# Kernel optimization log

Measured on AMD Instinct MI355X. Metric: run time of the kernel, lower is better.

Reference implementation:

```python
import jax, jax.numpy as jnp
import numpy as np
from jax import lax


def _forward(z_real, z_imag, dt, conv_w, conv_b, lin_w, lin_b,
             sc_w1, sc_b1, sc_w2, sc_b2, L_gen, diss_base, viscosity):
    B, T, C, H, W = z_real.shape
    Wf = W // 2 + 1
    x_mag = jnp.sqrt(z_real * z_real + z_imag * z_imag)  # |z|, (B,T,C,H,W)

    # ---- CFLTimeWarper ----
    v_proxy = x_mag.mean(axis=(3, 4), keepdims=True) + 1e-6      # (B,T,C,1,1)
    dt_max = 1.0 / (v_proxy * 10.0)                              # dx=1, max_velocity=10
    x_in = jnp.concatenate([z_real, z_imag], axis=2).reshape(B * T, 2 * C, H, W)
    h = lax.conv_general_dilated(x_in, conv_w, (1, 1), 'SAME',
                                 dimension_numbers=('NCHW', 'OIHW', 'NCHW'))
    h = jax.nn.silu(h + conv_b[None, :, None, None])
    pooled = h.mean(axis=(2, 3))                                 # AdaptiveAvgPool2d(1)
    alpha = jax.nn.sigmoid(pooled @ lin_w.T + lin_b).reshape(B, T, 1, 1, 1)
    dt_eff = alpha * jnp.minimum(dt, dt_max)                     # (B,T,C,1,1)

    # ---- LyapunovController (out_dim = 3C) ----
    ge = x_mag.mean(axis=(-2, -1))                               # (B,T,C)
    ctrl = jnp.tanh(jax.nn.silu(ge @ sc_w1.T + sc_b1) @ sc_w2.T + sc_b2)  # (B,T,3C)
    d_omega = ctrl[..., :C] * 0.1
    valve = ctrl[..., 2 * C:]
    omega_t = L_gen + d_omega                                    # (B,T,C)
    B_valve = jax.nn.sigmoid(valve) * 2.0                        # (B,T,C)

    # ---- spectral decay / rotation operators ----
    gamma_base = -jax.nn.softplus(diss_base)                     # (C,)
    nu = jax.nn.softplus(viscosity)
    ky = jnp.fft.fftfreq(H).astype(jnp.float32)
    kx = jnp.fft.rfftfreq(W).astype(jnp.float32)
    k_sq = kx[None, :] ** 2 + ky[:, None] ** 2                   # (H,Wf)
    gamma_k = gamma_base[:, None, None] - nu * k_sq[None]        # (C,H,Wf)
    gamma_term = gamma_k[None, None] * dt_eff                    # (B,T,C,H,Wf)
    omega_term = omega_t[..., None, None] * dt_eff               # (B,T,C,1,1)
    A_decay = jnp.exp(gamma_term)
    half = 0.5j * omega_term.astype(jnp.complex64)
    A_rot = (1.0 + half) / (1.0 - half)                          # Cayley rotation
    A_op = A_decay * A_rot                                       # (B,T,C,H,Wf) complex

    # ---- forward_spectral: complex input -> stack real/imag on batch ----
    u_in = jnp.concatenate([z_real, z_imag], axis=0)             # (2B,T,C,H,W)
    A_op = jnp.concatenate([A_op, A_op], axis=0)                 # (2B,T,C,H,Wf)
    Bv = jnp.concatenate([B_valve, B_valve], axis=0)             # (2B,T,C)
    z_fft = jnp.fft.rfft2(u_in, norm='ortho')                    # (2B,T,C,H,Wf)
    u_fft = z_fft * Bv[..., None, None]
    u_flat = jnp.transpose(u_fft, (0, 3, 4, 1, 2)).reshape(2 * B * H * Wf, T, C)
    A_flat = jnp.transpose(A_op, (0, 3, 4, 1, 2)).reshape(2 * B * H * Wf, T, C)
    return u_flat, A_flat, dt_eff


def setup_inputs() -> dict:
    key = jax.random.key(0)
    ks = jax.random.split(key, 10)
    B, T, C, H, W = 2, 8, 64, 128, 128
    z_real = jax.random.normal(ks[0], (B, T, C, H, W), jnp.float32)
    z_imag = jax.random.normal(ks[1], (B, T, C, H, W), jnp.float32)
    dt = jnp.ones((), jnp.float32)
    conv_w = jax.random.normal(ks[2], (C // 4, 2 * C, 3, 3), jnp.float32) * 0.05
    conv_b = jnp.zeros((C // 4,), jnp.float32)
    lin_w = jax.random.normal(ks[3], (1, C // 4), jnp.float32) * 0.05
    lin_b = jnp.zeros((1,), jnp.float32)
    sc_w1 = jax.random.normal(ks[4], (C // 2, C), jnp.float32) * 0.05
    sc_b1 = jnp.zeros((C // 2,), jnp.float32)
    sc_w2 = jax.random.normal(ks[5], (3 * C, C // 2), jnp.float32) * 0.05
    sc_b2 = jnp.zeros((3 * C,), jnp.float32)
    L_gen = jax.random.normal(ks[6], (C,), jnp.float32) * 0.01
    diss_base = jnp.zeros((C,), jnp.float32)
    viscosity = jnp.float32(0.001)
    return {"z_real": z_real, "z_imag": z_imag, "dt": dt,
            "conv_w": conv_w, "conv_b": conv_b, "lin_w": lin_w, "lin_b": lin_b,
            "sc_w1": sc_w1, "sc_b1": sc_b1, "sc_w2": sc_w2, "sc_b2": sc_b2,
            "L_gen": L_gen, "diss_base": diss_base, "viscosity": viscosity}


def reference(z_real, z_imag, dt, conv_w, conv_b, lin_w, lin_b,
              sc_w1, sc_b1, sc_w2, sc_b2, L_gen, diss_base, viscosity):
    return _forward(z_real, z_imag, dt, conv_w, conv_b, lin_w, lin_b,
                    sc_w1, sc_b1, sc_w2, sc_b2, L_gen, diss_base, viscosity)
```

## Files before the change

kernel.cpp:

```cpp
#include <hip/hip_runtime.h>
#include <math.h>

#define HW_ 16384

#define WS_GE    0
#define WS_POOL  1024
#define WS_DTEFF 17408
#define WS_ROTRE 18432
#define WS_ROTIM 19456
#define WS_BV    20480
#define WS_GB    21504
#define WS_NU    21568
__device__ float g_ws[22528];


struct Tw {
  float t0c, t0s;
  float c[6], s[6];
};

__device__ __forceinline__ void tw_init(int lane, Tw& tw) {
  sincospif(-(float)lane * (1.0f / 64.0f), &tw.t0s, &tw.t0c);
#pragma unroll
  for (int i = 0; i < 6; ++i) {
    int sp = 32 >> i;
    int j = lane & (sp - 1);
    float sv, cv;
    sincospif(-(float)j / (float)sp, &sv, &cv);
    bool bit = (lane & sp) != 0;
    tw.c[i] = bit ? cv : 1.0f;
    tw.s[i] = bit ? sv : 0.0f;
  }
}

__device__ __forceinline__ void fft128(int lane, float2& e0, float2& e1, const Tw& tw) {
  float ax = e0.x + e1.x, ay = e0.y + e1.y;
  float dx = e0.x - e1.x, dy = e0.y - e1.y;
  e0.x = ax; e0.y = ay;
  float t1x = dx * tw.t0c - dy * tw.t0s;
  float t1y = dx * tw.t0s + dy * tw.t0c;
  e1.x = t1x; e1.y = t1y;
#pragma unroll
  for (int i = 0; i < 6; ++i) {
    int sp = 32 >> i;
    bool bit = (lane & sp) != 0;
    float o0x = __shfl_xor(e0.x, sp, 64);
    float o0y = __shfl_xor(e0.y, sp, 64);
    float o1x = __shfl_xor(e1.x, sp, 64);
    float o1y = __shfl_xor(e1.y, sp, 64);
    float s0x = bit ? (o0x - e0.x) : (e0.x + o0x);
    float s0y = bit ? (o0y - e0.y) : (e0.y + o0y);
    float s1x = bit ? (o1x - e1.x) : (e1.x + o1x);
    float s1y = bit ? (o1y - e1.y) : (e1.y + o1y);
    e0.x = s0x * tw.c[i] - s0y * tw.s[i];
    e0.y = s0x * tw.s[i] + s0y * tw.c[i];
    e1.x = s1x * tw.c[i] - s1y * tw.s[i];
    e1.y = s1x * tw.s[i] + s1y * tw.c[i];
  }
}

__global__ __launch_bounds__(256) void k_rowfft2(
    const float* __restrict__ zsrc, const float* __restrict__ zother,
    float2* __restrict__ panel, int with_mag)
{
  __shared__ __align__(16) float2 Mr[65][34];
  __shared__ __align__(16) float2 Wb[4][128];
  __shared__ float redb[4];

  int n = blockIdx.x;
  int b = n >> 9, t = (n >> 6) & 7, c = n & 63;
  int tid = threadIdx.x, w = tid >> 6, lane = tid & 63;
  const float* pr = zsrc + (size_t)n * HW_;
  const float* po = zother + (size_t)n * HW_;
  Tw tw; tw_init(lane, tw);
  int k0 = (int)(__brev((unsigned)lane) >> 25);
  float msum = 0.0f;
  size_t base = ((size_t)((b * 8 + t) * 65)) * 8192 + (size_t)c * 128;

  for (int q = 0; q < 4; ++q) {
    for (int i = 0; i < 8; ++i) {
      int hl = w * 8 + i;
      int h = q * 32 + hl;
      float a0 = pr[h * 128 + lane];
      float a1 = pr[h * 128 + lane + 64];
      if (with_mag) {
        float b0 = po[h * 128 + lane];
        float b1 = po[h * 128 + lane + 64];
        msum += sqrtf(a0 * a0 + b0 * b0) + sqrtf(a1 * a1 + b1 * b1);
      }
      float2 e0 = make_float2(a0, 0.0f);
      float2 e1 = make_float2(a1, 0.0f);
      fft128(lane, e0, e1, tw);
      *(float4*)&Wb[w][k0] = make_float4(e0.x, e0.y, e1.x, e1.y);
      __syncthreads();
      Mr[lane][hl] = Wb[w][lane];
      if (lane == 0) Mr[64][hl] = Wb[w][64];
    }
    __syncthreads();
    for (int idx = tid; idx < 1040; idx += 256) {
      int f = idx * 2;
      int wf = f >> 5, hl = f & 31;
      float4 v = *(const float4*)&Mr[wf][hl];
      *(float4*)&panel[base + (size_t)wf * 8192 + q * 32 + hl] = v;
    }
    __syncthreads();
  }
  if (with_mag) {
#pragma unroll
    for (int off = 32; off; off >>= 1) msum += __shfl_down(msum, off, 64);
    if (lane == 0) redb[w] = msum;
    __syncthreads();
    if (tid == 0) g_ws[WS_GE + n] = redb[0] + redb[1] + redb[2] + redb[3];
  }
}

__global__ __launch_bounds__(256) void k_conv1(
    const float* __restrict__ zr, const float* __restrict__ zi,
    const float* __restrict__ conv_w, const float* __restrict__ conv_b)
{
  __shared__ float xs[18][24];
  __shared__ float redb[4][16];

  int bx = blockIdx.x;
  int n = bx >> 6, tsub = bx & 63;
  int ty0 = (tsub >> 3) * 16, tx0 = (tsub & 7) * 16;
  int tid = threadIdx.x;
  int py = tid >> 4, px = tid & 15;

  float acc[16];
#pragma unroll
  for (int i = 0; i < 16; ++i) acc[i] = 0.0f;

  for (int ci = 0; ci < 128; ++ci) {
    __syncthreads();
    const float* plane = ((ci < 64) ? zr : zi) + ((size_t)n * 64 + (ci & 63)) * HW_;
    for (int i = tid; i < 324; i += 256) {
      int r = i / 18, col = i - r * 18;
      int gy = ty0 - 1 + r, gx = tx0 - 1 + col;
      float v = 0.0f;
      if (gy >= 0 && gy < 128 && gx >= 0 && gx < 128) v = plane[gy * 128 + gx];
      xs[r][col] = v;
    }
    __syncthreads();
    float x0 = xs[py][px],     x1 = xs[py][px + 1],     x2 = xs[py][px + 2];
    float x3 = xs[py + 1][px], x4 = xs[py + 1][px + 1], x5 = xs[py + 1][px + 2];
    float x6 = xs[py + 2][px], x7 = xs[py + 2][px + 1], x8 = xs[py + 2][px + 2];
    const float* wci = conv_w + (size_t)ci * 9;
#pragma unroll
    for (int co = 0; co < 16; ++co) {
      const float* wp = wci + (size_t)co * 1152;
      acc[co] += x0 * wp[0] + x1 * wp[1] + x2 * wp[2]
               + x3 * wp[3] + x4 * wp[4] + x5 * wp[5]
               + x6 * wp[6] + x7 * wp[7] + x8 * wp[8];
    }
  }
  int w = tid >> 6, lane = tid & 63;
#pragma unroll
  for (int co = 0; co < 16; ++co) {
    float v = acc[co] + conv_b[co];
    v = v / (1.0f + expf(-v));
#pragma unroll
    for (int off = 32; off; off >>= 1) v += __shfl_down(v, off, 64);
    if (lane == 0) redb[w][co] = v;
  }
  __syncthreads();
  if (tid < 16) {
    g_ws[WS_POOL + bx * 16 + tid] = redb[0][tid] + redb[1][tid] + redb[2][tid] + redb[3][tid];
  }
}

__global__ __launch_bounds__(256) void k_ctrl(
    const float* __restrict__ dtp, const float* __restrict__ lin_w, const float* __restrict__ lin_b,
    const float* __restrict__ sc_w1, const float* __restrict__ sc_b1,
    const float* __restrict__ sc_w2, const float* __restrict__ sc_b2,
    const float* __restrict__ L_gen, const float* __restrict__ diss_base, const float* __restrict__ visc,
    float* __restrict__ out_dteff)
{
  __shared__ float geL[16][64];
  __shared__ float poolL[16][16];
  __shared__ float alphaL[16];
  __shared__ float hid[16][32];
  __shared__ float ctl[16][128];
  int tid = threadIdx.x;
  for (int i = tid; i < 1024; i += 256) geL[i >> 6][i & 63] = g_ws[WS_GE + i] * (1.0f / 16384.0f);
  {
    int nn = tid >> 4, co = tid & 15;
    float s = 0.0f;
    for (int tile = 0; tile < 64; ++tile) s += g_ws[WS_POOL + (nn * 64 + tile) * 16 + co];
    poolL[nn][co] = s * (1.0f / 16384.0f);
  }
  __syncthreads();
  if (tid < 16) {
    float s = lin_b[0];
    for (int co = 0; co < 16; ++co) s += poolL[tid][co] * lin_w[co];
    alphaL[tid] = 1.0f / (1.0f + expf(-s));
  }
  for (int i = tid; i < 512; i += 256) {
    int nn = i >> 5, j = i & 31;
    float s = sc_b1[j];
    for (int cc = 0; cc < 64; ++cc) s += geL[nn][cc] * sc_w1[j * 64 + cc];
    hid[nn][j] = s / (1.0f + expf(-s));
  }
  __syncthreads();
  for (int i = tid; i < 2048; i += 256) {
    int nn = i >> 7, kk = i & 127;
    int k = (kk < 64) ? kk : (kk + 64);
    float s = sc_b2[k];
    for (int j = 0; j < 32; ++j) s += hid[nn][j] * sc_w2[k * 32 + j];
    ctl[nn][kk] = tanhf(s);
  }
  __syncthreads();
  float dtv = dtp[0];
  for (int e = tid; e < 1024; e += 256) {
    int nn = e >> 6, cc = e & 63;
    float gem = geL[nn][cc];
    float dtmax = 1.0f / (10.0f * (gem + 1e-6f));
    float dte = alphaL[nn] * fminf(dtv, dtmax);
    float om = L_gen[cc] + 0.1f * ctl[nn][cc];
    float x = 0.5f * om * dte;
    float inv = 1.0f / (1.0f + x * x);
    g_ws[WS_DTEFF + e] = dte;
    g_ws[WS_ROTRE + e] = (1.0f - x * x) * inv;
    g_ws[WS_ROTIM + e] = 2.0f * x * inv;
    float vv = ctl[nn][64 + cc];
    g_ws[WS_BV + e] = 2.0f / (1.0f + expf(-vv));
    out_dteff[e] = dte;
  }
  if (tid < 64) g_ws[WS_GB + tid] = -log1pf(expf(diss_base[tid]));
  if (tid == 0) g_ws[WS_NU] = log1pf(expf(visc[0]));
}

__global__ __launch_bounds__(256) void k_colfft2(
    const float2* __restrict__ panel, float* __restrict__ outU, int ubbase)
{
  __shared__ __align__(16) float2 M2[32][132];
  __shared__ float fs[64];
  int bx = blockIdx.x;
  int b = bx / 520;
  int rem = bx - b * 520;
  int t = rem / 65;
  int wf = rem - t * 65;
  int ub = ubbase + b;
  int tid = threadIdx.x, w = tid >> 6, lane = tid & 63;
  Tw tw; tw_init(lane, tw);
  int k0 = (int)(__brev((unsigned)lane) >> 25);
  const float2* src = panel + (((size_t)(b * 8 + t)) * 65 + wf) * 8192;
  if (tid < 64) fs[tid] = g_ws[WS_BV + b * 512 + t * 64 + tid] * (1.0f / 128.0f);
  size_t ob = ((((size_t)ub * 128) * 65 + (size_t)wf) * 8 + (size_t)t) * 64;
  for (int q = 0; q < 2; ++q) {
    __syncthreads();
    for (int i = tid; i < 2048; i += 256) {
      float4 v = *(const float4*)&src[(size_t)q * 4096 + (size_t)i * 2];
      int f = i * 2;
      int cl = f >> 7, hh = f & 127;
      *(float4*)&M2[cl][hh] = v;
    }
    __syncthreads();
    for (int i = 0; i < 8; ++i) {
      int cl = w * 8 + i;
      float2 e0 = M2[cl][lane];
      float2 e1 = M2[cl][lane + 64];
      fft128(lane, e0, e1, tw);
      *(float4*)&M2[cl][k0] = make_float4(e0.x, e0.y, e1.x, e1.y);
    }
    __syncthreads();
    for (int idx = tid; idx < 2048; idx += 256) {
      int h = idx >> 4, cl2 = (idx & 15) * 2;
      int cc = q * 32 + cl2;
      float re0 = M2[cl2][h].x;
      float re1 = M2[cl2 + 1][h].x;
      float2 o = make_float2(re0 * fs[cc], re1 * fs[cc + 1]);
      *(float2*)&outU[ob + (size_t)h * 33280 + cc] = o;
    }
  }
}

__global__ __launch_bounds__(256) void k_awrite(float* __restrict__ outA)
{
  int bx = blockIdx.x;
  int h = bx / 65;
  int wf = bx - h * 65;
  float kxv = (float)wf * (1.0f / 128.0f);
  float kyf = (h < 64) ? (float)h : (float)(h - 128);
  float kyv = kyf * (1.0f / 128.0f);
  float ksq = kxv * kxv + kyv * kyv;
  float nu = g_ws[WS_NU];
  int tid = threadIdx.x;
  for (int e2 = tid; e2 < 512; e2 += 256) {
    int b = e2 >> 8, t = (e2 >> 5) & 7, cc = (e2 & 31) * 2;
    int e = b * 512 + t * 64 + cc;
    float gk0 = g_ws[WS_GB + cc] - nu * ksq;
    float gk1 = g_ws[WS_GB + cc + 1] - nu * ksq;
    float ad0 = expf(gk0 * g_ws[WS_DTEFF + e]);
    float ad1 = expf(gk1 * g_ws[WS_DTEFF + e + 1]);
    float2 vre = make_float2(ad0 * g_ws[WS_ROTRE + e], ad1 * g_ws[WS_ROTRE + e + 1]);
    size_t o1 = ((((size_t)(b * 128 + h)) * 65 + wf) * 8 + t) * 64 + cc;
    size_t o2 = o1 + 8519680ull;
    *(float2*)&outA[o1] = vre;
    *(float2*)&outA[o2] = vre;
  }
}

extern "C" void kernel_launch(void* const* d_in, const int* in_sizes, int n_in,
                              void* d_out, int out_size, void* d_ws, size_t ws_size,
                              hipStream_t stream)
{
  (void)in_sizes; (void)n_in; (void)d_ws; (void)ws_size;
  const float* zr     = (const float*)d_in[0];
  const float* zi     = (const float*)d_in[1];
  const float* dtp    = (const float*)d_in[2];
  const float* conv_w = (const float*)d_in[3];
  const float* conv_b = (const float*)d_in[4];
  const float* lin_w  = (const float*)d_in[5];
  const float* lin_b  = (const float*)d_in[6];
  const float* sc_w1  = (const float*)d_in[7];
  const float* sc_b1  = (const float*)d_in[8];
  const float* sc_w2  = (const float*)d_in[9];
  const float* sc_b2  = (const float*)d_in[10];
  const float* L_gen  = (const float*)d_in[11];
  const float* diss   = (const float*)d_in[12];
  const float* visc   = (const float*)d_in[13];

  float* out = (float*)d_out;
  size_t S = ((size_t)out_size - 1024) / 2;
  float* dt_out = out + (size_t)out_size - 1024;
  float2* panel = (float2*)(out + S);

  k_rowfft2<<<1024, 256, 0, stream>>>(zr, zi, panel, 1);
  k_conv1  <<<1024, 256, 0, stream>>>(zr, zi, conv_w, conv_b);
  k_ctrl   <<<1, 256, 0, stream>>>(dtp, lin_w, lin_b, sc_w1, sc_b1, sc_w2, sc_b2, L_gen, diss, visc, dt_out);
  k_colfft2<<<1040, 256, 0, stream>>>(panel, out, 0);
  k_rowfft2<<<1024, 256, 0, stream>>>(zi, zi, panel, 0);
  k_colfft2<<<1040, 256, 0, stream>>>(panel, out, 2);
  k_awrite <<<8320, 256, 0, stream>>>(out + S);
}
```

Baseline: 513.1 us.

## Pack real/imag row FFTs into one complex FFT, store bf16 panels, prefetch conv

The row FFT now transforms z_real + i*z_imag as one complex 128-point FFT and separates the two real-input spectra with the Hermitian split. This removes the second row-FFT launch and the second read of z_imag. The intermediate panels are stored as bf16 instead of fp32, which halves panel traffic between the row and column FFT kernels but loses precision in the spectral intermediates. The conv kernel also gains register prefetch of the next input-channel plane, occupancy launch bounds, and manual unrolling.

Measured after the change: 427.4 us. -16.7%, faster.

```diff
diff --git a/kernel.cpp b/kernel.cpp
--- a/kernel.cpp
+++ b/kernel.cpp
@@ -13,6 +13,15 @@
 #define WS_NU    21568
 __device__ float g_ws[22528];
 
+
+__device__ __forceinline__ unsigned short f2bf(float f) {
+  unsigned u = __float_as_uint(f);
+  u += 0x7fffu + ((u >> 16) & 1u);
+  return (unsigned short)(u >> 16);
+}
+__device__ __forceinline__ float bf2f(unsigned short h) {
+  return __uint_as_float((unsigned)h << 16);
+}
 
 struct Tw {
   float t0c, t0s;
@@ -59,19 +68,20 @@
   }
 }
 
-__global__ __launch_bounds__(256) void k_rowfft2(
-    const float* __restrict__ zsrc, const float* __restrict__ zother,
-    float2* __restrict__ panel, int with_mag)
+__global__ __launch_bounds__(256) void k_rowfftP(
+    const float* __restrict__ zr, const float* __restrict__ zi,
+    ushort2* __restrict__ panelR, ushort2* __restrict__ panelI)
 {
   __shared__ __align__(16) float2 Mr[65][34];
+  __shared__ __align__(16) float2 Mi[65][34];
   __shared__ __align__(16) float2 Wb[4][128];
   __shared__ float redb[4];
 
   int n = blockIdx.x;
   int b = n >> 9, t = (n >> 6) & 7, c = n & 63;
   int tid = threadIdx.x, w = tid >> 6, lane = tid & 63;
-  const float* pr = zsrc + (size_t)n * HW_;
-  const float* po = zother + (size_t)n * HW_;
+  const float* pr = zr + (size_t)n * HW_;
+  const float* pim = zi + (size_t)n * HW_;
   Tw tw; tw_init(lane, tw);
   int k0 = (int)(__brev((unsigned)lane) >> 25);
   float msum = 0.0f;
@@ -83,38 +93,45 @@
       int h = q * 32 + hl;
       float a0 = pr[h * 128 + lane];
       float a1 = pr[h * 128 + lane + 64];
-      if (with_mag) {
-        float b0 = po[h * 128 + lane];
-        float b1 = po[h * 128 + lane + 64];
-        msum += sqrtf(a0 * a0 + b0 * b0) + sqrtf(a1 * a1 + b1 * b1);
-      }
-      float2 e0 = make_float2(a0, 0.0f);
-      float2 e1 = make_float2(a1, 0.0f);
+      float b0 = pim[h * 128 + lane];
+      float b1 = pim[h * 128 + lane + 64];
+      msum += sqrtf(a0 * a0 + b0 * b0) + sqrtf(a1 * a1 + b1 * b1);
+      float2 e0 = make_float2(a0, b0);
+      float2 e1 = make_float2(a1, b1);
       fft128(lane, e0, e1, tw);
       *(float4*)&Wb[w][k0] = make_float4(e0.x, e0.y, e1.x, e1.y);
       __syncthreads();
-      Mr[lane][hl] = Wb[w][lane];
-      if (lane == 0) Mr[64][hl] = Wb[w][64];
+      float2 Zk = Wb[w][lane];
+      float2 Zm = Wb[w][(128 - lane) & 127];
+      Mr[lane][hl] = make_float2(0.5f * (Zk.x + Zm.x), 0.5f * (Zk.y - Zm.y));
+      Mi[lane][hl] = make_float2(0.5f * (Zk.y + Zm.y), 0.5f * (Zm.x - Zk.x));
+      if (lane == 0) {
+        float2 Z64 = Wb[w][64];
+        Mr[64][hl] = make_float2(Z64.x, 0.0f);
+        Mi[64][hl] = make_float2(Z64.y, 0.0f);
+      }
     }
     __syncthreads();
     for (int idx = tid; idx < 1040; idx += 256) {
       int f = idx * 2;
       int wf = f >> 5, hl = f & 31;
-      float4 v = *(const float4*)&Mr[wf][hl];
-      *(float4*)&panel[base + (size_t)wf * 8192 + q * 32 + hl] = v;
-    }
-    __syncthreads();
-  }
-  if (with_mag) {
+      float4 vr = *(const float4*)&Mr[wf][hl];
+      float4 vi = *(const float4*)&Mi[wf][hl];
+      ushort4 ur = make_ushort4(f2bf(vr.x), f2bf(vr.y), f2bf(vr.z), f2bf(vr.w));
+      ushort4 ui = make_ushort4(f2bf(vi.x), f2bf(vi.y), f2bf(vi.z), f2bf(vi.w));
+      *(ushort4*)&panelR[base + (size_t)wf * 8192 + q * 32 + hl] = ur;
+      *(ushort4*)&panelI[base + (size_t)wf * 8192 + q * 32 + hl] = ui;
+    }
+    __syncthreads();
+  }
 #pragma unroll
-    for (int off = 32; off; off >>= 1) msum += __shfl_down(msum, off, 64);
-    if (lane == 0) redb[w] = msum;
-    __syncthreads();
-    if (tid == 0) g_ws[WS_GE + n] = redb[0] + redb[1] + redb[2] + redb[3];
-  }
-}
-
-__global__ __launch_bounds__(256) void k_conv1(
+  for (int off = 32; off; off >>= 1) msum += __shfl_down(msum, off, 64);
+  if (lane == 0) redb[w] = msum;
+  __syncthreads();
+  if (tid == 0) g_ws[WS_GE + n] = redb[0] + redb[1] + redb[2] + redb[3];
+}
+
+__global__ __launch_bounds__(256, 4) void k_conv1(
     const float* __restrict__ zr, const float* __restrict__ zi,
     const float* __restrict__ conv_w, const float* __restrict__ conv_b)
 {
@@ -127,42 +144,61 @@
   int tid = threadIdx.x;
   int py = tid >> 4, px = tid & 15;
 
-  float acc[16];
-#pragma unroll
-  for (int i = 0; i < 16; ++i) acc[i] = 0.0f;
+  int r0 = tid / 18, c0 = tid - r0 * 18;
+  int gy0 = ty0 - 1 + r0, gx0 = tx0 - 1 + c0;
+  bool ok0 = (gy0 >= 0) && (gy0 < 128) && (gx0 >= 0) && (gx0 < 128);
+  int i1 = tid + 256;
+  int r1 = i1 / 18, c1 = i1 - r1 * 18;
+  int gy1 = ty0 - 1 + r1, gx1 = tx0 - 1 + c1;
+  bool has1 = (i1 < 324);
+  bool ok1 = has1 && (gy1 >= 0) && (gy1 < 128) && (gx1 >= 0) && (gx1 < 128);
+  int off0 = gy0 * 128 + gx0;
+  int off1 = gy1 * 128 + gx1;
+
+  const float* pbr = zr + (size_t)n * 64 * HW_;
+  const float* pbi = zi + (size_t)n * 64 * HW_;
+
+  float acc0=0,acc1=0,acc2=0,acc3=0,acc4=0,acc5=0,acc6=0,acc7=0;
+  float acc8=0,acc9=0,acc10=0,acc11=0,acc12=0,acc13=0,acc14=0,acc15=0;
+
+  float nxt0 = ok0 ? pbr[off0] : 0.0f;
+  float nxt1 = ok1 ? pbr[off1] : 0.0f;
 
   for (int ci = 0; ci < 128; ++ci) {
     __syncthreads();
-    const float* plane = ((ci < 64) ? zr : zi) + ((size_t)n * 64 + (ci & 63)) * HW_;
-    for (int i = tid; i < 324; i += 256) {
-      int r = i / 18, col = i - r * 18;
-      int gy = ty0 - 1 + r, gx = tx0 - 1 + col;
-      float v = 0.0f;
-      if (gy >= 0 && gy < 128 && gx >= 0 && gx < 128) v = plane[gy * 128 + gx];
-      xs[r][col] = v;
-    }
-    __syncthreads();
-    float x0 = xs[py][px],     x1 = xs[py][px + 1],     x2 = xs[py][px + 2];
-    float x3 = xs[py + 1][px], x4 = xs[py + 1][px + 1], x5 = xs[py + 1][px + 2];
-    float x6 = xs[py + 2][px], x7 = xs[py + 2][px + 1], x8 = xs[py + 2][px + 2];
+    xs[r0][c0] = nxt0;
+    if (has1) xs[r1][c1] = nxt1;
+    __syncthreads();
+    if (ci + 1 < 128) {
+      const float* pl = ((ci + 1) < 64 ? pbr : pbi) + (size_t)((ci + 1) & 63) * HW_;
+      nxt0 = ok0 ? pl[off0] : 0.0f;
+      nxt1 = ok1 ? pl[off1] : 0.0f;
+    }
+    volatile const float* xb = &xs[0][0];
+    int a = py * 24 + px;
+    float x0 = xb[a],      x1 = xb[a + 1],  x2 = xb[a + 2];
+    float x3 = xb[a + 24], x4 = xb[a + 25], x5 = xb[a + 26];
+    float x6 = xb[a + 48], x7 = xb[a + 49], x8 = xb[a + 50];
     const float* wci = conv_w + (size_t)ci * 9;
-#pragma unroll
-    for (int co = 0; co < 16; ++co) {
-      const float* wp = wci + (size_t)co * 1152;
-      acc[co] += x0 * wp[0] + x1 * wp[1] + x2 * wp[2]
-               + x3 * wp[3] + x4 * wp[4] + x5 * wp[5]
-               + x6 * wp[6] + x7 * wp[7] + x8 * wp[8];
-    }
-  }
+#define CO_STEP(K) { const float* wp = wci + (size_t)(K) * 1152;                      \
+    acc##K += x0*wp[0] + x1*wp[1] + x2*wp[2] + x3*wp[3] + x4*wp[4] + x5*wp[5]         \
+            + x6*wp[6] + x7*wp[7] + x8*wp[8]; }
+    CO_STEP(0)  CO_STEP(1)  CO_STEP(2)  CO_STEP(3)
+    CO_STEP(4)  CO_STEP(5)  CO_STEP(6)  CO_STEP(7)
+    CO_STEP(8)  CO_STEP(9)  CO_STEP(10) CO_STEP(11)
+    CO_STEP(12) CO_STEP(13) CO_STEP(14) CO_STEP(15)
+#undef CO_STEP
+  }
+
   int w = tid >> 6, lane = tid & 63;
-#pragma unroll
-  for (int co = 0; co < 16; ++co) {
-    float v = acc[co] + conv_b[co];
-    v = v / (1.0f + expf(-v));
-#pragma unroll
-    for (int off = 32; off; off >>= 1) v += __shfl_down(v, off, 64);
-    if (lane == 0) redb[w][co] = v;
-  }
+#define POOL(K) { float v = acc##K + conv_b[K]; v = v / (1.0f + expf(-v));            \
+    _Pragma("unroll") for (int off = 32; off; off >>= 1) v += __shfl_down(v, off, 64);\
+    if (lane == 0) redb[w][K] = v; }
+  POOL(0)  POOL(1)  POOL(2)  POOL(3)
+  POOL(4)  POOL(5)  POOL(6)  POOL(7)
+  POOL(8)  POOL(9)  POOL(10) POOL(11)
+  POOL(12) POOL(13) POOL(14) POOL(15)
+#undef POOL
   __syncthreads();
   if (tid < 16) {
     g_ws[WS_POOL + bx * 16 + tid] = redb[0][tid] + redb[1][tid] + redb[2][tid] + redb[3][tid];
@@ -231,7 +267,7 @@
 }
 
 __global__ __launch_bounds__(256) void k_colfft2(
-    const float2* __restrict__ panel, float* __restrict__ outU, int ubbase)
+    const ushort2* __restrict__ panel, float* __restrict__ outU, int ubbase)
 {
   __shared__ __align__(16) float2 M2[32][132];
   __shared__ float fs[64];
@@ -244,16 +280,16 @@
   int tid = threadIdx.x, w = tid >> 6, lane = tid & 63;
   Tw tw; tw_init(lane, tw);
   int k0 = (int)(__brev((unsigned)lane) >> 25);
-  const float2* src = panel + (((size_t)(b * 8 + t)) * 65 + wf) * 8192;
+  const ushort2* src = panel + (((size_t)(b * 8 + t)) * 65 + wf) * 8192;
   if (tid < 64) fs[tid] = g_ws[WS_BV + b * 512 + t * 64 + tid] * (1.0f / 128.0f);
   size_t ob = ((((size_t)ub * 128) * 65 + (size_t)wf) * 8 + (size_t)t) * 64;
   for (int q = 0; q < 2; ++q) {
     __syncthreads();
     for (int i = tid; i < 2048; i += 256) {
-      float4 v = *(const float4*)&src[(size_t)q * 4096 + (size_t)i * 2];
+      ushort4 raw = *(const ushort4*)&src[(size_t)q * 4096 + (size_t)i * 2];
       int f = i * 2;
       int cl = f >> 7, hh = f & 127;
-      *(float4*)&M2[cl][hh] = v;
+      *(float4*)&M2[cl][hh] = make_float4(bf2f(raw.x), bf2f(raw.y), bf2f(raw.z), bf2f(raw.w));
     }
     __syncthreads();
     for (int i = 0; i < 8; ++i) {
@@ -324,13 +360,13 @@
   float* out = (float*)d_out;
   size_t S = ((size_t)out_size - 1024) / 2;
   float* dt_out = out + (size_t)out_size - 1024;
-  float2* panel = (float2*)(out + S);
-
-  k_rowfft2<<<1024, 256, 0, stream>>>(zr, zi, panel, 1);
+  ushort2* panelR = (ushort2*)(out + S);
+  ushort2* panelI = panelR + 8519680ull;
+
+  k_rowfftP<<<1024, 256, 0, stream>>>(zr, zi, panelR, panelI);
   k_conv1  <<<1024, 256, 0, stream>>>(zr, zi, conv_w, conv_b);
   k_ctrl   <<<1, 256, 0, stream>>>(dtp, lin_w, lin_b, sc_w1, sc_b1, sc_w2, sc_b2, L_gen, diss, visc, dt_out);
-  k_colfft2<<<1040, 256, 0, stream>>>(panel, out, 0);
-  k_rowfft2<<<1024, 256, 0, stream>>>(zi, zi, panel, 0);
-  k_colfft2<<<1040, 256, 0, stream>>>(panel, out, 2);
+  k_colfft2<<<1040, 256, 0, stream>>>(panelR, out, 0);
+  k_colfft2<<<1040, 256, 0, stream>>>(panelI, out, 2);
   k_awrite <<<8320, 256, 0, stream>>>(out + S);
 }
```
